# Optimization experiments

Measured on AMD Instinct MI355X. Metric: run time of the kernel, lower is better.

## Reference

```python
import jax, jax.numpy as jnp
import numpy as np

N_NODES = 100000
N_EDGES = 1000000
F_IN = 64
F_HID = 64
F_OUT = 2
NUM_GRAPHS = 64


def setup_inputs() -> dict:
    key = jax.random.key(0)
    ks = jax.random.split(key, 8)
    x = jax.random.normal(ks[0], (N_NODES, F_IN), dtype=jnp.float32)
    edge_index = jax.random.randint(ks[1], (2, N_EDGES), 0, N_NODES, dtype=jnp.int32)
    batch = jnp.sort(jax.random.randint(ks[2], (N_NODES,), 0, NUM_GRAPHS, dtype=jnp.int32))
    s1 = 1.0 / np.sqrt(F_IN)
    s2 = 1.0 / np.sqrt(F_HID)
    W1 = jax.random.normal(ks[3], (F_IN, F_HID), dtype=jnp.float32) * s1
    W2 = jax.random.normal(ks[4], (F_HID, F_HID), dtype=jnp.float32) * s2
    W3 = jax.random.normal(ks[5], (F_HID, F_HID), dtype=jnp.float32) * s2
    Wlin = jax.random.normal(ks[6], (F_HID, F_OUT), dtype=jnp.float32) * s2
    return {
        "x": x, "edge_index": edge_index, "batch": batch,
        "W1": W1, "b1": jnp.zeros((F_HID,), jnp.float32),
        "W2": W2, "b2": jnp.zeros((F_HID,), jnp.float32),
        "W3": W3, "b3": jnp.zeros((F_HID,), jnp.float32),
        "Wlin": Wlin, "blin": jnp.zeros((F_OUT,), jnp.float32),
    }


def _gcn_norm(edge_index, n_nodes):
    # add self-loops, compute symmetric D^-1/2 (A+I) D^-1/2 edge weights
    loops = jnp.arange(n_nodes, dtype=edge_index.dtype)
    src = jnp.concatenate([edge_index[0], loops])  # message source j
    dst = jnp.concatenate([edge_index[1], loops])  # aggregation target i
    deg = jax.ops.segment_sum(jnp.ones_like(dst, dtype=jnp.float32), dst,
                              num_segments=n_nodes)
    dinv = jnp.where(deg > 0, jax.lax.rsqrt(deg), 0.0)
    norm = dinv[src] * dinv[dst]  # [E+N]
    return src, dst, norm


def _gcn_conv(h, W, b, src, dst, norm, n_nodes):
    h = h @ W                                    # [N, F] dense transform first (PyG order)
    msg = h[src] * norm[:, None]                 # gather + scale  [E+N, F]
    agg = jax.ops.segment_sum(msg, dst, num_segments=n_nodes)
    return agg + b


def reference(x, edge_index, batch, W1, b1, W2, b2, W3, b3, Wlin, blin):
    n = x.shape[0]
    src, dst, norm = _gcn_norm(edge_index, n)
    h = jax.nn.relu(_gcn_conv(x, W1, b1, src, dst, norm, n))
    h = jax.nn.relu(_gcn_conv(h, W2, b2, src, dst, norm, n))
    h = _gcn_conv(h, W3, b3, src, dst, norm, n)
    # global mean pool over graphs
    sums = jax.ops.segment_sum(h, batch, num_segments=NUM_GRAPHS)        # [G, F]
    cnts = jax.ops.segment_sum(jnp.ones((n,), jnp.float32), batch,
                               num_segments=NUM_GRAPHS)
    pooled = sums / jnp.maximum(cnts, 1.0)[:, None]
    # dropout(p=0.1) is identity in eval mode
    return pooled @ Wlin + blin
```

## Files before the change

### kernel.cpp

```cpp
#include <hip/hip_runtime.h>

#define FDIM 64

typedef unsigned short u16;
typedef unsigned int u32;
typedef unsigned long long u64;
typedef float v2f __attribute__((ext_vector_type(2)));

__device__ __forceinline__ u16 f2bf(float x) {
    unsigned int u = __float_as_uint(x);
    return (u16)((u + 0x7fff + ((u >> 16) & 1)) >> 16);
}
__device__ __forceinline__ float bf2f(u16 h) {
    return __uint_as_float(((unsigned int)h) << 16);
}
__device__ __forceinline__ u32 pk_fp8x4(float a, float b, float c, float d) {
    u32 p = __builtin_amdgcn_cvt_pk_fp8_f32(a, b, 0, false);
    p = __builtin_amdgcn_cvt_pk_fp8_f32(c, d, p, true);
    return p;
}


template <bool SCALE>
__device__ __forceinline__ void mm_compute(
    u32* __restrict__ t, const int* __restrict__ cnt, int n, int r0,
    float (*__restrict__ As)[FDIM + 1], const float* __restrict__ Ws)
{
    int tid = threadIdx.x;
    int rq = tid >> 4;
    int cq = tid & 15;
    float acc[4][4];
    #pragma unroll
    for (int i = 0; i < 4; ++i)
        #pragma unroll
        for (int j = 0; j < 4; ++j) acc[i][j] = 0.f;

    const float4* Ws4 = (const float4*)Ws;
    #pragma unroll 4
    for (int k = 0; k < FDIM; ++k) {
        float4 w = Ws4[k * 16 + cq];
        float a[4];
        #pragma unroll
        for (int i = 0; i < 4; ++i) a[i] = As[rq * 4 + i][k];
        #pragma unroll
        for (int i = 0; i < 4; ++i) {
            acc[i][0] = fmaf(a[i], w.x, acc[i][0]);
            acc[i][1] = fmaf(a[i], w.y, acc[i][1]);
            acc[i][2] = fmaf(a[i], w.z, acc[i][2]);
            acc[i][3] = fmaf(a[i], w.w, acc[i][3]);
        }
    }

    #pragma unroll
    for (int i = 0; i < 4; ++i) {
        int R = r0 + rq * 4 + i;
        if (R < n) {
            float sc = 1.0f;
            if (SCALE) sc = rsqrtf((float)cnt[R] + 1.0f);
            t[(size_t)R * 16 + cq] =
                pk_fp8x4(acc[i][0] * sc, acc[i][1] * sc,
                         acc[i][2] * sc, acc[i][3] * sc);
        }
    }
}


__device__ __forceinline__ void mm_compute_bf16(
    u32* __restrict__ t, const int* __restrict__ cnt, int n, int r0,
    u32 (*__restrict__ Asb)[33], const float* __restrict__ Ws)
{
    int tid = threadIdx.x;
    int rq = tid >> 4;
    int cq = tid & 15;
    float acc[4][4];
    #pragma unroll
    for (int i = 0; i < 4; ++i)
        #pragma unroll
        for (int j = 0; j < 4; ++j) acc[i][j] = 0.f;

    const float4* Ws4 = (const float4*)Ws;
    #pragma unroll 4
    for (int k2 = 0; k2 < FDIM / 2; ++k2) {
        float4 w0 = Ws4[(2 * k2) * 16 + cq];
        float4 w1 = Ws4[(2 * k2 + 1) * 16 + cq];
        float a0[4], a1[4];
        #pragma unroll
        for (int i = 0; i < 4; ++i) {
            u32 pk = Asb[rq * 4 + i][k2];
            a0[i] = bf2f((u16)(pk & 0xffff));
            a1[i] = bf2f((u16)(pk >> 16));
        }
        #pragma unroll
        for (int i = 0; i < 4; ++i) {
            acc[i][0] = fmaf(a0[i], w0.x, acc[i][0]);
            acc[i][1] = fmaf(a0[i], w0.y, acc[i][1]);
            acc[i][2] = fmaf(a0[i], w0.z, acc[i][2]);
            acc[i][3] = fmaf(a0[i], w0.w, acc[i][3]);
            acc[i][0] = fmaf(a1[i], w1.x, acc[i][0]);
            acc[i][1] = fmaf(a1[i], w1.y, acc[i][1]);
            acc[i][2] = fmaf(a1[i], w1.z, acc[i][2]);
            acc[i][3] = fmaf(a1[i], w1.w, acc[i][3]);
        }
    }

    #pragma unroll
    for (int i = 0; i < 4; ++i) {
        int R = r0 + rq * 4 + i;
        if (R < n) {
            float sc = rsqrtf((float)cnt[R] + 1.0f);
            t[(size_t)R * 16 + cq] =
                pk_fp8x4(acc[i][0] * sc, acc[i][1] * sc,
                         acc[i][2] * sc, acc[i][3] * sc);
        }
    }
}


__global__ __launch_bounds__(256) void k_hist_mm(
    const int* __restrict__ dst, int* __restrict__ hpart,
    u32* __restrict__ zA, u32* __restrict__ zB,
    const float* __restrict__ x, const float* __restrict__ W1,
    u32* __restrict__ t, int n, int E, int nbuk, int hist_blocks)
{
    __shared__ float As[64][FDIM + 1];
    __shared__ float Ws[FDIM * FDIM];
    __shared__ int h[1024];

    int tid = threadIdx.x, blk = blockIdx.x;
    if ((int)blk < hist_blocks) {
        if (blk == 0 && tid < 16) { zA[tid] = 0u; zB[tid] = 0u; }
        for (int b = tid; b < nbuk; b += 256) h[b] = 0;
        __syncthreads();
        int stride = hist_blocks * 256;
        for (int e = blk * 256 + tid; e < E; e += stride)
            atomicAdd(&h[dst[e] >> 8], 1);
        __syncthreads();
        for (int b = tid; b < nbuk; b += 256) hpart[b * 256 + blk] = h[b];
        return;
    }

    int r0 = (blk - hist_blocks) * 64;
    #pragma unroll
    for (int i = 0; i < 4; ++i)
        ((float4*)Ws)[tid + 256 * i] = ((const float4*)W1)[tid + 256 * i];
    #pragma unroll
    for (int i = 0; i < 4; ++i) {
        int idx = tid + 256 * i;
        int r = idx >> 4;
        int kq = idx & 15;
        float4 v = make_float4(0.f, 0.f, 0.f, 0.f);
        int R = r0 + r;
        if (R < n) v = ((const float4*)x)[(size_t)R * 16 + kq];
        As[r][kq * 4 + 0] = v.x;
        As[r][kq * 4 + 1] = v.y;
        As[r][kq * 4 + 2] = v.z;
        As[r][kq * 4 + 3] = v.w;
    }
    __syncthreads();
    mm_compute<false>(t, nullptr, n, r0, As, Ws);
}

__global__ __launch_bounds__(256) void k_scan_a(
    int* __restrict__ hpart, int* __restrict__ bb)
{
    __shared__ int s[256];
    int b = blockIdx.x;
    int tid = threadIdx.x;
    int v = hpart[(size_t)b * 256 + tid];
    s[tid] = v;
    __syncthreads();
    #pragma unroll
    for (int off = 1; off < 256; off <<= 1) {
        int w = (tid >= off) ? s[tid - off] : 0;
        __syncthreads();
        s[tid] += w;
        __syncthreads();
    }
    hpart[(size_t)b * 256 + tid] = s[tid] - v;
    if (tid == 255) bb[b] = s[255];
}

__global__ __launch_bounds__(256) void k_scan_b(
    int* __restrict__ bb, int nbuk)
{
    __shared__ int s[512];
    int tid = threadIdx.x;
    s[tid]       = (tid < nbuk) ? bb[tid] : 0;
    s[tid + 256] = (tid + 256 < nbuk) ? bb[tid + 256] : 0;
    __syncthreads();
    #pragma unroll
    for (int off = 1; off < 512; off <<= 1) {
        int a0 = (tid >= off) ? s[tid - off] : 0;
        int a1 = (tid + 256 >= off) ? s[tid + 256 - off] : 0;
        __syncthreads();
        s[tid] += a0;
        s[tid + 256] += a1;
        __syncthreads();
    }
    int e0 = (tid == 0) ? 0 : s[tid - 1];
    int e1 = s[tid + 255];
    if (tid < nbuk) bb[tid] = e0;
    if (tid + 256 < nbuk) bb[tid + 256] = e1;
    if (tid == 255) bb[nbuk] = s[511];
}

__global__ __launch_bounds__(256) void k_scatter(
    const int* __restrict__ src, const int* __restrict__ dst,
    const int* __restrict__ hpart, const int* __restrict__ bb,
    u64* __restrict__ ebuf, int E, int nbuk)
{
    __shared__ int cur[1024];
    int tid = threadIdx.x, blk = blockIdx.x;
    for (int b = tid; b < nbuk; b += 256)
        cur[b] = hpart[(size_t)b * 256 + blk] + bb[b];
    __syncthreads();
    int stride = gridDim.x * 256;
    for (int e = blk * 256 + tid; e < E; e += stride) {
        int d = dst[e], s = src[e];
        int p = atomicAdd(&cur[d >> 8], 1);
        ebuf[p] = ((u64)(u32)d << 32) | (u32)s;
    }
}

__global__ __launch_bounds__(256) void k_build(
    const u64* __restrict__ ebuf, const int* __restrict__ bb,
    int* __restrict__ cnt, int* __restrict__ rptr, int* __restrict__ csr,
    int n)
{
    __shared__ int cnt_l[256], scn[256], cur[256];
    int tid = threadIdx.x;
    int b = blockIdx.x;
    int node0 = b << 8;
    int nn = n - node0; if (nn > 256) nn = 256;
    int e0 = bb[b], e1 = bb[b + 1];

    cnt_l[tid] = 0;
    __syncthreads();
    for (int e = e0 + tid; e < e1; e += 256)
        atomicAdd(&cnt_l[(int)(ebuf[e] >> 32) & 255], 1);
    __syncthreads();
    int v = cnt_l[tid];
    scn[tid] = v;
    __syncthreads();
    #pragma unroll
    for (int off = 1; off < 256; off <<= 1) {
        int w = (tid >= off) ? scn[tid - off] : 0;
        __syncthreads();
        scn[tid] += w;
        __syncthreads();
    }
    int excl = scn[tid] - v;
    if (tid < nn) {
        cnt[node0 + tid]  = v;
        rptr[node0 + tid] = e0 + excl;
    }
    cur[tid] = e0 + excl;
    __syncthreads();
    for (int e = e0 + tid; e < e1; e += 256) {
        u64 pk = ebuf[e];
        int local = (int)(pk >> 32) & 255;
        int p = atomicAdd(&cur[local], 1);
        csr[p] = (int)(u32)(pk & 0xffffffffu);
    }
}


template <bool SCALED>
__device__ __forceinline__ float4 agg_node(
    int i, const int* __restrict__ cnt, const int* __restrict__ rptr,
    const int* __restrict__ csr, const u32* __restrict__ t,
    int li, int nbase)
{
    int dg = cnt[i];
    float di = rsqrtf((float)dg + 1.0f);
    int m = dg;

    u32 sp = t[(size_t)i * 16 + li];
    v2f s0 = __builtin_amdgcn_cvt_pk_f32_fp8(sp, false);
    v2f s1 = __builtin_amdgcn_cvt_pk_f32_fp8(sp, true);
    float4 A0, A1, A2, A3;
    if (SCALED) {
        A0 = make_float4(s0.x, s0.y, s1.x, s1.y);
    } else {
        A0 = make_float4(s0.x * di, s0.y * di, s1.x * di, s1.y * di);
    }
    A1 = make_float4(0.f, 0.f, 0.f, 0.f);
    A2 = make_float4(0.f, 0.f, 0.f, 0.f);
    A3 = make_float4(0.f, 0.f, 0.f, 0.f);

    const int* row = csr + rptr[i];

    for (int c0 = 0; c0 < m; c0 += 16) {
        int cm = m - c0; if (cm > 16) cm = 16;
        int sv = -1; float dvv = 0.f;
        if (li < cm) {
            sv = __builtin_nontemporal_load(&row[c0 + li]);
            if (!SCALED) dvv = rsqrtf((float)cnt[sv] + 1.0f);
        }
        int jv[16]; float dj[16]; u32 v[16];
        #pragma unroll
        for (int u = 0; u < 16; ++u) {
            jv[u] = __shfl(sv, nbase + u);
            if (!SCALED) dj[u] = __shfl(dvv, nbase + u);
        }
        #pragma unroll
        for (int u = 0; u < 16; ++u)
            v[u] = t[(long long)jv[u] * 16 + li];
        #pragma unroll
        for (int u = 0; u < 16; ++u) {
            v2f x0 = __builtin_amdgcn_cvt_pk_f32_fp8(v[u], false);
            v2f x1 = __builtin_amdgcn_cvt_pk_f32_fp8(v[u], true);
            float4* Ap = (u & 3) == 0 ? &A0 : (u & 3) == 1 ? &A1 :
                         (u & 3) == 2 ? &A2 : &A3;
            if (SCALED) {
                Ap->x += x0.x; Ap->y += x0.y;
                Ap->z += x1.x; Ap->w += x1.y;
            } else {
                Ap->x = fmaf(x0.x, dj[u], Ap->x);
                Ap->y = fmaf(x0.y, dj[u], Ap->y);
                Ap->z = fmaf(x1.x, dj[u], Ap->z);
                Ap->w = fmaf(x1.y, dj[u], Ap->w);
            }
        }
    }

    float4 O;
    O.x = ((A0.x + A1.x) + (A2.x + A3.x)) * di;
    O.y = ((A0.y + A1.y) + (A2.y + A3.y)) * di;
    O.z = ((A0.z + A1.z) + (A2.z + A3.z)) * di;
    O.w = ((A0.w + A1.w) + (A2.w + A3.w)) * di;
    return O;
}


template <bool SCALED_IN>
__global__ __launch_bounds__(256) void k_aggmm(
    const int* __restrict__ cnt, const int* __restrict__ rptr,
    const int* __restrict__ csr, const u32* __restrict__ tin,
    const float* __restrict__ Wm, const float* __restrict__ bias,
    u32* __restrict__ tout, int n)
{
    __shared__ u32 Asb[64][33];
    __shared__ float Ws[FDIM * FDIM];
    int tid = threadIdx.x;
    #pragma unroll
    for (int i = 0; i < 4; ++i)
        ((float4*)Ws)[tid + 256 * i] = ((const float4*)Wm)[tid + 256 * i];

    int r0 = blockIdx.x * 64;
    int group = tid >> 4;
    int li = tid & 15;
    int nbase = ((tid & 63) >> 4) << 4;
    float4 b = ((const float4*)bias)[li];

    #pragma unroll 1
    for (int r = 0; r < 4; ++r) {
        int row = r * 16 + group;
        int i = r0 + row;
        float4 v = make_float4(0.f, 0.f, 0.f, 0.f);
        if (i < n) {
            float4 O = agg_node<SCALED_IN>(i, cnt, rptr, csr, tin, li, nbase);
            v.x = fmaxf(O.x + b.x, 0.f);
            v.y = fmaxf(O.y + b.y, 0.f);
            v.z = fmaxf(O.z + b.z, 0.f);
            v.w = fmaxf(O.w + b.w, 0.f);
        }
        Asb[row][li * 2 + 0] = ((u32)f2bf(v.x)) | (((u32)f2bf(v.y)) << 16);
        Asb[row][li * 2 + 1] = ((u32)f2bf(v.z)) | (((u32)f2bf(v.w)) << 16);
    }
    __syncthreads();
    mm_compute_bf16(tout, cnt, n, r0, Asb, Ws);
}


__global__ __launch_bounds__(256) void k_agg_pool(
    const int* __restrict__ cnt, const int* __restrict__ rptr,
    const int* __restrict__ csr, const u32* __restrict__ t,
    const int* __restrict__ batch, float* __restrict__ partial,
    int n, int npart)
{
    int g = blockIdx.x / npart;
    int part = blockIdx.x - g * npart;
    int tid = threadIdx.x;

    int lo = 0, hi = n;
    while (lo < hi) { int mid = (lo + hi) >> 1; if (batch[mid] < g) lo = mid + 1; else hi = mid; }
    int start = lo;
    hi = n;
    while (lo < hi) { int mid = (lo + hi) >> 1; if (batch[mid] <= g) lo = mid + 1; else hi = mid; }
    int end = lo;

    int group = tid >> 4;
    int li = tid & 15;
    int nbase = ((tid & 63) >> 4) << 4;

    float4 acc = make_float4(0.f, 0.f, 0.f, 0.f);
    for (int i = start + part * 16 + group; i < end; i += npart * 16) {
        float4 O = agg_node<true>(i, cnt, rptr, csr, t, li, nbase);
        acc.x += O.x; acc.y += O.y; acc.z += O.z; acc.w += O.w;
    }

    __shared__ float4 red[16][16];
    red[group][li] = acc;
    __syncthreads();
    if (tid < 16) {
        float4 s = make_float4(0.f, 0.f, 0.f, 0.f);
        #pragma unroll
        for (int q = 0; q < 16; ++q) {
            s.x += red[q][tid].x; s.y += red[q][tid].y;
            s.z += red[q][tid].z; s.w += red[q][tid].w;
        }
        ((float4*)partial)[((size_t)g * npart + part) * 16 + tid] = s;
    }
}


__global__ __launch_bounds__(64) void k_pool2(
    const float* __restrict__ partial, const int* __restrict__ batch,
    const float* __restrict__ b3, const float* __restrict__ Wlin,
    const float* __restrict__ blin, float* __restrict__ out,
    int n, int fout, int npart)
{
    int g = blockIdx.x;
    int tid = threadIdx.x;

    int lo = 0, hi = n;
    while (lo < hi) { int mid = (lo + hi) >> 1; if (batch[mid] < g) lo = mid + 1; else hi = mid; }
    int start = lo;
    hi = n;
    while (lo < hi) { int mid = (lo + hi) >> 1; if (batch[mid] <= g) lo = mid + 1; else hi = mid; }
    int cg = lo - start;

    __shared__ float pooled[64];
    float v = 0.f;
    for (int p = 0; p < npart; ++p)
        v += partial[((size_t)g * npart + p) * 64 + tid];
    pooled[tid] = (cg > 0) ? (v / (float)cg + b3[tid]) : 0.f;
    __syncthreads();
    if (tid < fout) {
        float o = blin[tid];
        for (int k = 0; k < 64; ++k) o += pooled[k] * Wlin[k * fout + tid];
        out[(size_t)g * fout + tid] = o;
    }
}


extern "C" void kernel_launch(void* const* d_in, const int* in_sizes, int n_in,
                              void* d_out, int out_size, void* d_ws, size_t ws_size,
                              hipStream_t stream) {
    const float* x     = (const float*)d_in[0];
    const int*   ei    = (const int*)d_in[1];
    const int*   batch = (const int*)d_in[2];
    const float* W1 = (const float*)d_in[3];
    const float* b1 = (const float*)d_in[4];
    const float* W2 = (const float*)d_in[5];
    const float* b2 = (const float*)d_in[6];
    const float* W3 = (const float*)d_in[7];
    const float* b3 = (const float*)d_in[8];
    const float* Wl = (const float*)d_in[9];
    const float* bl = (const float*)d_in[10];

    int n = in_sizes[0] / 64;
    int E = in_sizes[1] / 2;
    int fout = in_sizes[10];
    int ngraphs = out_size / fout;

    const int* srcp = ei;
    const int* dstp = ei + E;

    const int npart = 16;
    int nbuk = (n + 255) >> 8;

    u64* ebuf = (u64*)d_ws;
    int* csr  = (int*)(ebuf + (size_t)E);
    int* cnt  = csr + (size_t)E;
    int* rptr = cnt + n;
    int* bb   = rptr + n;
    int* hpart = bb + (nbuk + 1);
    u32* zA  = (u32*)(hpart + (size_t)nbuk * 256);
    u32* tA  = zA + 16;
    u32* zB  = tA + (size_t)n * 16;
    u32* tB  = zB + 16;
    float* ppool = (float*)(tB + (size_t)n * 16);

    int mm_blocks = (n + 63) / 64;
    int hist_blocks = 256;

    k_hist_mm<<<hist_blocks + mm_blocks, 256, 0, stream>>>(
        dstp, hpart, zA, zB, x, W1, tA, n, E, nbuk, hist_blocks);
    k_scan_a<<<nbuk, 256, 0, stream>>>(hpart, bb);
    k_scan_b<<<1, 256, 0, stream>>>(bb, nbuk);
    k_scatter<<<256, 256, 0, stream>>>(srcp, dstp, hpart, bb, ebuf, E, nbuk);
    k_build<<<nbuk, 256, 0, stream>>>(ebuf, bb, cnt, rptr, csr, n);

    k_aggmm<false><<<mm_blocks, 256, 0, stream>>>(cnt, rptr, csr, tA, W2, b1, tB, n);
    k_aggmm<true><<<mm_blocks, 256, 0, stream>>>(cnt, rptr, csr, tB, W3, b2, tA, n);
    k_agg_pool<<<ngraphs * npart, 256, 0, stream>>>(
        cnt, rptr, csr, tA, batch, ppool, n, npart);
    k_pool2<<<ngraphs, 64, 0, stream>>>(ppool, batch, b3, Wl, bl,
                                        (float*)d_out, n, fout, npart);
}
```

Baseline: 244.3 us.

## Split fp8 feature table into two half-width arrays and aggregate in two passes

The fp8 node feature table is stored as two separate 32-byte-per-node halves instead of one 64-byte row. Aggregation runs two passes, one per half, with each 16-lane group handling two neighbors at a time over 8 lanes and combining the partial sums with a cross-lane shuffle. The aim is a smaller gathered table per pass, so each pass's working set fits better in L2/MALL and random gathers hit cache more often. In exchange, the CSR index reads and degree lookups are done twice, and half the lanes only write results.

```diff
diff --git a/kernel.cpp b/kernel.cpp
--- a/kernel.cpp
+++ b/kernel.cpp
@@ -23,7 +23,8 @@
 
 template <bool SCALE>
 __device__ __forceinline__ void mm_compute(
-    u32* __restrict__ t, const int* __restrict__ cnt, int n, int r0,
+    u32* __restrict__ tLo, u32* __restrict__ tHi,
+    const int* __restrict__ cnt, int n, int r0,
     float (*__restrict__ As)[FDIM + 1], const float* __restrict__ Ws)
 {
     int tid = threadIdx.x;
@@ -57,16 +58,18 @@
         if (R < n) {
             float sc = 1.0f;
             if (SCALE) sc = rsqrtf((float)cnt[R] + 1.0f);
-            t[(size_t)R * 16 + cq] =
-                pk_fp8x4(acc[i][0] * sc, acc[i][1] * sc,
-                         acc[i][2] * sc, acc[i][3] * sc);
+            u32 pk = pk_fp8x4(acc[i][0] * sc, acc[i][1] * sc,
+                              acc[i][2] * sc, acc[i][3] * sc);
+            if (cq < 8) tLo[(size_t)R * 8 + cq] = pk;
+            else        tHi[(size_t)R * 8 + cq - 8] = pk;
         }
     }
 }
 
 
 __device__ __forceinline__ void mm_compute_bf16(
-    u32* __restrict__ t, const int* __restrict__ cnt, int n, int r0,
+    u32* __restrict__ tLo, u32* __restrict__ tHi,
+    const int* __restrict__ cnt, int n, int r0,
     u32 (*__restrict__ Asb)[33], const float* __restrict__ Ws)
 {
     int tid = threadIdx.x;
@@ -108,9 +111,10 @@
         int R = r0 + rq * 4 + i;
         if (R < n) {
             float sc = rsqrtf((float)cnt[R] + 1.0f);
-            t[(size_t)R * 16 + cq] =
-                pk_fp8x4(acc[i][0] * sc, acc[i][1] * sc,
-                         acc[i][2] * sc, acc[i][3] * sc);
+            u32 pk = pk_fp8x4(acc[i][0] * sc, acc[i][1] * sc,
+                              acc[i][2] * sc, acc[i][3] * sc);
+            if (cq < 8) tLo[(size_t)R * 8 + cq] = pk;
+            else        tHi[(size_t)R * 8 + cq - 8] = pk;
         }
     }
 }
@@ -118,9 +122,10 @@
 
 __global__ __launch_bounds__(256) void k_hist_mm(
     const int* __restrict__ dst, int* __restrict__ hpart,
-    u32* __restrict__ zA, u32* __restrict__ zB,
+    u32* __restrict__ tALo, u32* __restrict__ tAHi,
+    u32* __restrict__ tBLo, u32* __restrict__ tBHi,
     const float* __restrict__ x, const float* __restrict__ W1,
-    u32* __restrict__ t, int n, int E, int nbuk, int hist_blocks)
+    int n, int E, int nbuk, int hist_blocks)
 {
     __shared__ float As[64][FDIM + 1];
     __shared__ float Ws[FDIM * FDIM];
@@ -128,7 +133,10 @@
 
     int tid = threadIdx.x, blk = blockIdx.x;
     if ((int)blk < hist_blocks) {
-        if (blk == 0 && tid < 16) { zA[tid] = 0u; zB[tid] = 0u; }
+        if (blk == 0 && tid < 16) {
+            (tALo - 16)[tid] = 0u; (tAHi - 16)[tid] = 0u;
+            (tBLo - 16)[tid] = 0u; (tBHi - 16)[tid] = 0u;
+        }
         for (int b = tid; b < nbuk; b += 256) h[b] = 0;
         __syncthreads();
         int stride = hist_blocks * 256;
@@ -157,7 +165,7 @@
         As[r][kq * 4 + 3] = v.w;
     }
     __syncthreads();
-    mm_compute<false>(t, nullptr, n, r0, As, Ws);
+    mm_compute<false>(tALo, tAHi, nullptr, n, r0, As, Ws);
 }
 
 __global__ __launch_bounds__(256) void k_scan_a(
@@ -266,29 +274,18 @@
 
 
 template <bool SCALED>
-__device__ __forceinline__ float4 agg_node(
+__device__ __forceinline__ float4 agg_node_half(
     int i, const int* __restrict__ cnt, const int* __restrict__ rptr,
-    const int* __restrict__ csr, const u32* __restrict__ t,
-    int li, int nbase)
+    const int* __restrict__ csr, const u32* __restrict__ th,
+    int li, int nbase, int s8, int f8)
 {
     int dg = cnt[i];
     float di = rsqrtf((float)dg + 1.0f);
     int m = dg;
-
-    u32 sp = t[(size_t)i * 16 + li];
-    v2f s0 = __builtin_amdgcn_cvt_pk_f32_fp8(sp, false);
-    v2f s1 = __builtin_amdgcn_cvt_pk_f32_fp8(sp, true);
-    float4 A0, A1, A2, A3;
-    if (SCALED) {
-        A0 = make_float4(s0.x, s0.y, s1.x, s1.y);
-    } else {
-        A0 = make_float4(s0.x * di, s0.y * di, s1.x * di, s1.y * di);
-    }
-    A1 = make_float4(0.f, 0.f, 0.f, 0.f);
-    A2 = make_float4(0.f, 0.f, 0.f, 0.f);
-    A3 = make_float4(0.f, 0.f, 0.f, 0.f);
-
     const int* row = csr + rptr[i];
+
+    float4 A0 = make_float4(0.f, 0.f, 0.f, 0.f);
+    float4 A1 = A0, A2 = A0, A3 = A0;
 
     for (int c0 = 0; c0 < m; c0 += 16) {
         int cm = m - c0; if (cm > 16) cm = 16;
@@ -297,17 +294,17 @@
             sv = __builtin_nontemporal_load(&row[c0 + li]);
             if (!SCALED) dvv = rsqrtf((float)cnt[sv] + 1.0f);
         }
-        int jv[16]; float dj[16]; u32 v[16];
-        #pragma unroll
-        for (int u = 0; u < 16; ++u) {
-            jv[u] = __shfl(sv, nbase + u);
-            if (!SCALED) dj[u] = __shfl(dvv, nbase + u);
-        }
-        #pragma unroll
-        for (int u = 0; u < 16; ++u)
-            v[u] = t[(long long)jv[u] * 16 + li];
-        #pragma unroll
-        for (int u = 0; u < 16; ++u) {
+        int jv[8]; float dj[8]; u32 v[8];
+        #pragma unroll
+        for (int u = 0; u < 8; ++u) {
+            jv[u] = __shfl(sv, nbase + 2 * u + s8);
+            if (!SCALED) dj[u] = __shfl(dvv, nbase + 2 * u + s8);
+        }
+        #pragma unroll
+        for (int u = 0; u < 8; ++u)
+            v[u] = th[(long long)jv[u] * 8 + f8];
+        #pragma unroll
+        for (int u = 0; u < 8; ++u) {
             v2f x0 = __builtin_amdgcn_cvt_pk_f32_fp8(v[u], false);
             v2f x1 = __builtin_amdgcn_cvt_pk_f32_fp8(v[u], true);
             float4* Ap = (u & 3) == 0 ? &A0 : (u & 3) == 1 ? &A1 :
@@ -324,21 +321,37 @@
         }
     }
 
-    float4 O;
-    O.x = ((A0.x + A1.x) + (A2.x + A3.x)) * di;
-    O.y = ((A0.y + A1.y) + (A2.y + A3.y)) * di;
-    O.z = ((A0.z + A1.z) + (A2.z + A3.z)) * di;
-    O.w = ((A0.w + A1.w) + (A2.w + A3.w)) * di;
-    return O;
+    float4 A;
+    A.x = (A0.x + A1.x) + (A2.x + A3.x);
+    A.y = (A0.y + A1.y) + (A2.y + A3.y);
+    A.z = (A0.z + A1.z) + (A2.z + A3.z);
+    A.w = (A0.w + A1.w) + (A2.w + A3.w);
+    A.x += __shfl_xor(A.x, 8);
+    A.y += __shfl_xor(A.y, 8);
+    A.z += __shfl_xor(A.z, 8);
+    A.w += __shfl_xor(A.w, 8);
+
+    u32 sp = th[(size_t)i * 8 + f8];
+    v2f s0 = __builtin_amdgcn_cvt_pk_f32_fp8(sp, false);
+    v2f s1 = __builtin_amdgcn_cvt_pk_f32_fp8(sp, true);
+    if (SCALED) {
+        A.x += s0.x; A.y += s0.y; A.z += s1.x; A.w += s1.y;
+    } else {
+        A.x = fmaf(s0.x, di, A.x); A.y = fmaf(s0.y, di, A.y);
+        A.z = fmaf(s1.x, di, A.z); A.w = fmaf(s1.y, di, A.w);
+    }
+    A.x *= di; A.y *= di; A.z *= di; A.w *= di;
+    return A;
 }
 
 
 template <bool SCALED_IN>
 __global__ __launch_bounds__(256) void k_aggmm(
     const int* __restrict__ cnt, const int* __restrict__ rptr,
-    const int* __restrict__ csr, const u32* __restrict__ tin,
+    const int* __restrict__ csr,
+    const u32* __restrict__ tinLo, const u32* __restrict__ tinHi,
     const float* __restrict__ Wm, const float* __restrict__ bias,
-    u32* __restrict__ tout, int n)
+    u32* __restrict__ toutLo, u32* __restrict__ toutHi, int n)
 {
     __shared__ u32 Asb[64][33];
     __shared__ float Ws[FDIM * FDIM];
@@ -351,31 +364,43 @@
     int group = tid >> 4;
     int li = tid & 15;
     int nbase = ((tid & 63) >> 4) << 4;
-    float4 b = ((const float4*)bias)[li];
+    int s8 = li >> 3;
+    int f8 = li & 7;
 
     #pragma unroll 1
-    for (int r = 0; r < 4; ++r) {
-        int row = r * 16 + group;
-        int i = r0 + row;
-        float4 v = make_float4(0.f, 0.f, 0.f, 0.f);
-        if (i < n) {
-            float4 O = agg_node<SCALED_IN>(i, cnt, rptr, csr, tin, li, nbase);
-            v.x = fmaxf(O.x + b.x, 0.f);
-            v.y = fmaxf(O.y + b.y, 0.f);
-            v.z = fmaxf(O.z + b.z, 0.f);
-            v.w = fmaxf(O.w + b.w, 0.f);
-        }
-        Asb[row][li * 2 + 0] = ((u32)f2bf(v.x)) | (((u32)f2bf(v.y)) << 16);
-        Asb[row][li * 2 + 1] = ((u32)f2bf(v.z)) | (((u32)f2bf(v.w)) << 16);
-    }
-    __syncthreads();
-    mm_compute_bf16(tout, cnt, n, r0, Asb, Ws);
+    for (int h = 0; h < 2; ++h) {
+        const u32* th = h ? tinHi : tinLo;
+        float4 b = ((const float4*)bias)[h * 8 + f8];
+        #pragma unroll 1
+        for (int r = 0; r < 4; ++r) {
+            int row = r * 16 + group;
+            int i = r0 + row;
+            float4 v = make_float4(0.f, 0.f, 0.f, 0.f);
+            if (i < n) {
+                float4 O = agg_node_half<SCALED_IN>(
+                    i, cnt, rptr, csr, th, li, nbase, s8, f8);
+                v.x = fmaxf(O.x + b.x, 0.f);
+                v.y = fmaxf(O.y + b.y, 0.f);
+                v.z = fmaxf(O.z + b.z, 0.f);
+                v.w = fmaxf(O.w + b.w, 0.f);
+            }
+            if (s8 == 0) {
+                Asb[row][h * 16 + f8 * 2 + 0] =
+                    ((u32)f2bf(v.x)) | (((u32)f2bf(v.y)) << 16);
+                Asb[row][h * 16 + f8 * 2 + 1] =
+                    ((u32)f2bf(v.z)) | (((u32)f2bf(v.w)) << 16);
+            }
+        }
+    }
+    __syncthreads();
+    mm_compute_bf16(toutLo, toutHi, cnt, n, r0, Asb, Ws);
 }
 
 
 __global__ __launch_bounds__(256) void k_agg_pool(
     const int* __restrict__ cnt, const int* __restrict__ rptr,
-    const int* __restrict__ csr, const u32* __restrict__ t,
+    const int* __restrict__ csr,
+    const u32* __restrict__ tLo, const u32* __restrict__ tHi,
     const int* __restrict__ batch, float* __restrict__ partial,
     int n, int npart)
 {
@@ -393,15 +418,22 @@
     int group = tid >> 4;
     int li = tid & 15;
     int nbase = ((tid & 63) >> 4) << 4;
-
-    float4 acc = make_float4(0.f, 0.f, 0.f, 0.f);
-    for (int i = start + part * 16 + group; i < end; i += npart * 16) {
-        float4 O = agg_node<true>(i, cnt, rptr, csr, t, li, nbase);
-        acc.x += O.x; acc.y += O.y; acc.z += O.z; acc.w += O.w;
-    }
+    int s8 = li >> 3;
+    int f8 = li & 7;
 
     __shared__ float4 red[16][16];
-    red[group][li] = acc;
+
+    #pragma unroll 1
+    for (int h = 0; h < 2; ++h) {
+        const u32* th = h ? tHi : tLo;
+        float4 acc = make_float4(0.f, 0.f, 0.f, 0.f);
+        for (int i = start + part * 16 + group; i < end; i += npart * 16) {
+            float4 O = agg_node_half<true>(
+                i, cnt, rptr, csr, th, li, nbase, s8, f8);
+            acc.x += O.x; acc.y += O.y; acc.z += O.z; acc.w += O.w;
+        }
+        if (s8 == 0) red[group][h * 8 + f8] = acc;
+    }
     __syncthreads();
     if (tid < 16) {
         float4 s = make_float4(0.f, 0.f, 0.f, 0.f);
@@ -477,26 +509,28 @@
     int* rptr = cnt + n;
     int* bb   = rptr + n;
     int* hpart = bb + (nbuk + 1);
-    u32* zA  = (u32*)(hpart + (size_t)nbuk * 256);
-    u32* tA  = zA + 16;
-    u32* zB  = tA + (size_t)n * 16;
-    u32* tB  = zB + 16;
-    float* ppool = (float*)(tB + (size_t)n * 16);
+    u32* tALo = (u32*)(hpart + (size_t)nbuk * 256) + 16;
+    u32* tAHi = tALo + (size_t)n * 8 + 16;
+    u32* tBLo = tAHi + (size_t)n * 8 + 16;
+    u32* tBHi = tBLo + (size_t)n * 8 + 16;
+    float* ppool = (float*)(tBHi + (size_t)n * 8);
 
     int mm_blocks = (n + 63) / 64;
     int hist_blocks = 256;
 
     k_hist_mm<<<hist_blocks + mm_blocks, 256, 0, stream>>>(
-        dstp, hpart, zA, zB, x, W1, tA, n, E, nbuk, hist_blocks);
+        dstp, hpart, tALo, tAHi, tBLo, tBHi, x, W1, n, E, nbuk, hist_blocks);
     k_scan_a<<<nbuk, 256, 0, stream>>>(hpart, bb);
     k_scan_b<<<1, 256, 0, stream>>>(bb, nbuk);
     k_scatter<<<256, 256, 0, stream>>>(srcp, dstp, hpart, bb, ebuf, E, nbuk);
     k_build<<<nbuk, 256, 0, stream>>>(ebuf, bb, cnt, rptr, csr, n);
 
-    k_aggmm<false><<<mm_blocks, 256, 0, stream>>>(cnt, rptr, csr, tA, W2, b1, tB, n);
-    k_aggmm<true><<<mm_blocks, 256, 0, stream>>>(cnt, rptr, csr, tB, W3, b2, tA, n);
+    k_aggmm<false><<<mm_blocks, 256, 0, stream>>>(
+        cnt, rptr, csr, tALo, tAHi, W2, b1, tBLo, tBHi, n);
+    k_aggmm<true><<<mm_blocks, 256, 0, stream>>>(
+        cnt, rptr, csr, tBLo, tBHi, W3, b2, tALo, tAHi, n);
     k_agg_pool<<<ngraphs * npart, 256, 0, stream>>>(
-        cnt, rptr, csr, tA, batch, ppool, n, npart);
+        cnt, rptr, csr, tALo, tAHi, batch, ppool, n, npart);
     k_pool2<<<ngraphs, 64, 0, stream>>>(ppool, batch, b3, Wl, bl,
                                         (float*)d_out, n, fout, npart);
 }
```

New measurement: 290.1 us. +18.7%, slower.
